# Kernel tuning notes

Hardware: AMD Instinct MI355X
Metric: run time of the kernel (lower is better)

The kernel has to match this reference:

```python
import jax, jax.numpy as jnp
import numpy as np

B, N, C, H, E = 16, 512, 128, 8, 131072
Nn = B * N
Dh = C // H
EPS = 1e-5


def setup_inputs() -> dict:
    key = jax.random.key(0)
    ks = jax.random.split(key, 16)
    s = C ** -0.5
    x = jax.random.normal(ks[0], (Nn, C), dtype=jnp.float32)
    edge_index = jax.random.randint(ks[1], (2, E), 0, Nn)
    batch = jnp.arange(Nn) // N  # B equal-sized graphs, sorted
    attn_bias = jax.random.normal(ks[2], (B, N, N, H), dtype=jnp.float32)
    return {
        "x": x,
        "edge_index": edge_index,
        "batch": batch,
        "attn_bias": attn_bias,
        "conv_w": jax.random.normal(ks[3], (C, C)) * s,
        "conv_b": jnp.zeros((C,)),
        "wq": jax.random.normal(ks[4], (C, C)) * s,
        "bq": jnp.zeros((C,)),
        "wk": jax.random.normal(ks[5], (C, C)) * s,
        "bk": jnp.zeros((C,)),
        "wv": jax.random.normal(ks[6], (C, C)) * s,
        "bv": jnp.zeros((C,)),
        "wo": jax.random.normal(ks[7], (C, C)) * s,
        "bo": jnp.zeros((C,)),
        "w1": jax.random.normal(ks[8], (C, 2 * C)) * s,
        "b1": jnp.zeros((2 * C,)),
        "w2": jax.random.normal(ks[9], (2 * C, C)) * (2 * C) ** -0.5,
        "b2": jnp.zeros((C,)),
        "g1": jnp.ones((C,)), "be1": jnp.zeros((C,)),
        "g2": jnp.ones((C,)), "be2": jnp.zeros((C,)),
        "g3": jnp.ones((C,)), "be3": jnp.zeros((C,)),
    }


def _bn(h, g, b):
    # BatchNorm1d over the node dimension (training-mode batch statistics)
    mu = h.mean(axis=0)
    var = h.var(axis=0)  # biased, matches torch normalization
    return g * (h - mu) * jax.lax.rsqrt(var + EPS) + b


def reference(x, edge_index, batch, attn_bias,
              conv_w, conv_b, wq, bq, wk, bk, wv, bv, wo, bo,
              w1, b1, w2, b2, g1, be1, g2, be2, g3, be3):
    n_nodes, ch = x.shape
    bsz, n_max, _, heads = attn_bias.shape
    dh = ch // heads

    # ---- GCN conv (self loops + symmetric norm) -> dropout(0) + residual + norm1
    loops = jnp.arange(n_nodes)
    src = jnp.concatenate([edge_index[0], loops])
    dst = jnp.concatenate([edge_index[1], loops])
    deg = jax.ops.segment_sum(jnp.ones_like(src, dtype=x.dtype), dst, num_segments=n_nodes)
    dinv = jax.lax.rsqrt(jnp.maximum(deg, 1.0))
    xw = x @ conv_w
    msg = xw[src] * (dinv[src] * dinv[dst])[:, None]
    hconv = jax.ops.segment_sum(msg, dst, num_segments=n_nodes) + conv_b
    h1 = _bn(hconv + x, g1, be1)

    # ---- dense batch (equal-sized sorted graphs -> pure reshape, mask all-valid)
    xd = x.reshape(bsz, n_max, ch)
    q = ((xd @ wq + bq) * (dh ** -0.5)).reshape(bsz, n_max, heads, dh)
    k = (xd @ wk + bk).reshape(bsz, n_max, heads, dh)
    v = (xd @ wv + bv).reshape(bsz, n_max, heads, dh)
    scores = jnp.einsum('bqhd,bkhd->bqkh', q, k) + attn_bias  # [B,N,N,H]
    probs = jax.nn.softmax(scores, axis=2)
    att = jnp.einsum('bqkh,bkhd->bqhd', probs, v).reshape(bsz, n_max, ch)
    att = att @ wo + bo
    h2 = _bn(att.reshape(n_nodes, ch) + x, g2, be2)

    # ---- combine branches, MLP with residual, norm3
    out = h1 + h2
    mlp = jax.nn.relu(out @ w1 + b1) @ w2 + b2
    return _bn(out + mlp, g3, be3)
```

## Files before the change

### kernel.cpp

```cpp
#include <hip/hip_runtime.h>
#include <cstddef>

#define NN 8192
#define CC 128


__global__ __launch_bounds__(256) void count_deg_int_k(const int* __restrict__ dst, int* degi, int E) {
  int i = blockIdx.x * 256 + threadIdx.x;
  if (i < E) atomicAdd(&degi[dst[i]], 1);
}

__global__ __launch_bounds__(256) void dinv_k(const int* __restrict__ degi, float* __restrict__ dinv, int n) {
  int i = blockIdx.x * 256 + threadIdx.x;
  if (i < n) dinv[i] = rsqrtf((float)(degi[i] + 1));
}

__global__ __launch_bounds__(256) void scan_k(const int* __restrict__ degi, int* __restrict__ rowstart,
                                              int* __restrict__ cursor) {
  __shared__ int partial[256];
  int t = threadIdx.x;
  int base = t * 32;
  int local[32];
  int s = 0;
#pragma unroll
  for (int i = 0; i < 32; ++i) { local[i] = s; s += degi[base + i]; }
  partial[t] = s;
  __syncthreads();
  for (int off = 1; off < 256; off <<= 1) {
    int v = (t >= off) ? partial[t - off] : 0;
    __syncthreads();
    partial[t] += v;
    __syncthreads();
  }
  int offset = partial[t] - s;
#pragma unroll
  for (int i = 0; i < 32; ++i) {
    rowstart[base + i] = offset + local[i];
    cursor[base + i] = offset + local[i];
  }
  if (t == 255) rowstart[NN] = offset + s;
}

__global__ __launch_bounds__(256) void bucket_k(const int* __restrict__ src, const int* __restrict__ dst,
    int* __restrict__ cursor, int* __restrict__ col, int E) {
  int e = blockIdx.x * 256 + threadIdx.x;
  if (e >= E) return;
  int d = dst[e];
  int pos = atomicAdd(&cursor[d], 1);
  col[pos] = src[e];
}

__global__ __launch_bounds__(256) void gather_k(const int* __restrict__ rowstart, const int* __restrict__ col,
    const float* __restrict__ xw, const float* __restrict__ dinv, const float* __restrict__ cb,
    const float* __restrict__ x, float* __restrict__ h1) {
  int d = blockIdx.x * 2 + (threadIdx.x >> 7);
  int c = threadIdx.x & 127;
  int j0 = rowstart[d], j1 = rowstart[d + 1];
  float dd = dinv[d];
  float sum = 0.f;
  int s_next = (j0 < j1) ? col[j0] : 0;
  for (int j = j0; j < j1; ++j) {
    int s = s_next;
    if (j + 1 < j1) s_next = col[j + 1];
    sum += xw[(size_t)s * CC + c] * dinv[s];
  }
  sum *= dd;
  int idx = d * CC + c;
  sum += xw[idx] * dd * dd;
  h1[idx] = sum + cb[c] + x[idx];
}


__global__ __launch_bounds__(256) void bn_stats_k(const float* __restrict__ X,
    float* __restrict__ sums, float* __restrict__ sumsq) {
  int t = threadIdx.x;
  int c = t & 127, rg = t >> 7;
  int r0 = blockIdx.x * 64;
  float s = 0.f, sq = 0.f;
  for (int i = 0; i < 32; ++i) {
    float v = X[(size_t)(r0 + rg + 2 * i) * CC + c];
    s += v; sq += v * v;
  }
  atomicAdd(&sums[c], s);
  atomicAdd(&sumsq[c], sq);
}

__global__ void bn_finalize_k(const float* sums, const float* sumsq, const float* g, const float* be,
                              float* scale, float* shift) {
  int c = threadIdx.x;
  float mu = sums[c] * (1.0f / NN);
  float var = sumsq[c] * (1.0f / NN) - mu * mu;
  float sc = g[c] * rsqrtf(var + 1e-5f);
  scale[c] = sc;
  shift[c] = be[c] - mu * sc;
}

__global__ __launch_bounds__(256) void combine_k(const float* __restrict__ h1, const float* __restrict__ h2,
    const float* __restrict__ sc0, const float* __restrict__ sh0,
    const float* __restrict__ sc1, const float* __restrict__ sh1, float* __restrict__ out) {
  int idx = blockIdx.x * 256 + threadIdx.x;
  int c = idx & 127;
  out[idx] = sc0[c] * h1[idx] + sh0[c] + sc1[c] * h2[idx] + sh1[c];
}

__global__ __launch_bounds__(256) void bn_apply_k(const float* __restrict__ h, const float* __restrict__ sc,
    const float* __restrict__ sh, float* __restrict__ out) {
  int idx = blockIdx.x * 256 + threadIdx.x;
  int c = idx & 127;
  out[idx] = sc[c] * h[idx] + sh[c];
}

__global__ __launch_bounds__(256) void gemm_k(const float* __restrict__ A, const float* __restrict__ W,
    const float* __restrict__ bias, const float* __restrict__ resid, float* __restrict__ out,
    int M, int N, int K, float scale, int relu) {
  __shared__ float As[64 * 128];
  __shared__ float Ws[128 * 64];
  int t = threadIdx.x;
  int ty = t >> 4, tx = t & 15;
  int row0 = blockIdx.x * 64, n0 = blockIdx.y * 64;
  float acc[4][4] = {};
  for (int kc = 0; kc < K; kc += 128) {
#pragma unroll
    for (int j = 0; j < 8; ++j) {
      int f = t + 256 * j;
      int r = f >> 5, c4 = f & 31;
      *(float4*)(As + r * 128 + c4 * 4) = *(const float4*)(A + (size_t)(row0 + r) * K + kc + c4 * 4);
    }
#pragma unroll
    for (int j = 0; j < 8; ++j) {
      int f = t + 256 * j;
      int kr = f >> 4, c4 = f & 15;
      *(float4*)(Ws + kr * 64 + c4 * 4) = *(const float4*)(W + (size_t)(kc + kr) * N + n0 + c4 * 4);
    }
    __syncthreads();
    for (int k0 = 0; k0 < 128; k0 += 4) {
      float a[4][4], b[4][4];
#pragma unroll
      for (int i = 0; i < 4; ++i) {
        float4 t4 = *(const float4*)(As + (4 * ty + i) * 128 + k0);
        a[i][0] = t4.x; a[i][1] = t4.y; a[i][2] = t4.z; a[i][3] = t4.w;
      }
#pragma unroll
      for (int kk = 0; kk < 4; ++kk) {
        float4 t4 = *(const float4*)(Ws + (k0 + kk) * 64 + 4 * tx);
        b[kk][0] = t4.x; b[kk][1] = t4.y; b[kk][2] = t4.z; b[kk][3] = t4.w;
      }
#pragma unroll
      for (int kk = 0; kk < 4; ++kk)
#pragma unroll
        for (int i = 0; i < 4; ++i)
#pragma unroll
          for (int j = 0; j < 4; ++j)
            acc[i][j] += a[i][kk] * b[kk][j];
    }
    __syncthreads();
  }
  float4 bv = make_float4(0.f, 0.f, 0.f, 0.f);
  if (bias) bv = *(const float4*)(bias + n0 + 4 * tx);
#pragma unroll
  for (int i = 0; i < 4; ++i) {
    float4 r;
    r.x = (acc[i][0] + bv.x) * scale;
    r.y = (acc[i][1] + bv.y) * scale;
    r.z = (acc[i][2] + bv.z) * scale;
    r.w = (acc[i][3] + bv.w) * scale;
    if (relu) { r.x = fmaxf(r.x, 0.f); r.y = fmaxf(r.y, 0.f); r.z = fmaxf(r.z, 0.f); r.w = fmaxf(r.w, 0.f); }
    size_t o = (size_t)(row0 + 4 * ty + i) * N + n0 + 4 * tx;
    if (resid) {
      float4 rv = *(const float4*)(resid + o);
      r.x += rv.x; r.y += rv.y; r.z += rv.z; r.w += rv.w;
    }
    *(float4*)(out + o) = r;
  }
}

__global__ __launch_bounds__(256) void attn_k(const float* __restrict__ Q, const float* __restrict__ K,
    const float* __restrict__ V, const float* __restrict__ bias, float* __restrict__ out) {
  __shared__ float Ks[64 * 128];
  __shared__ float Vs[64 * 128];
  const int t = threadIdx.x;
  const int b = blockIdx.x >> 4;
  const int qt = blockIdx.x & 15;
  const int q = t >> 3;
  const int h = t & 7;
  const int node = b * 512 + qt * 32 + q;

  float qf[16];
  {
    const float4* qp = (const float4*)(Q + (size_t)node * CC + h * 16);
    float4 q0 = qp[0], q1 = qp[1], q2 = qp[2], q3 = qp[3];
    qf[0] = q0.x; qf[1] = q0.y; qf[2] = q0.z; qf[3] = q0.w;
    qf[4] = q1.x; qf[5] = q1.y; qf[6] = q1.z; qf[7] = q1.w;
    qf[8] = q2.x; qf[9] = q2.y; qf[10] = q2.z; qf[11] = q2.w;
    qf[12] = q3.x; qf[13] = q3.y; qf[14] = q3.z; qf[15] = q3.w;
  }
  float m = -INFINITY, l = 0.f;
  float acc[16];
#pragma unroll
  for (int d = 0; d < 16; ++d) acc[d] = 0.f;

  const float* brow = bias + (size_t)node * 4096 + h;
  float bb_cur[8], bb_nxt[8];
#pragma unroll
  for (int j = 0; j < 8; ++j) bb_cur[j] = brow[j * 8];
#pragma unroll
  for (int j = 0; j < 8; ++j) bb_nxt[j] = 0.f;

  const size_t kbase = (size_t)b * 512 * CC;
  for (int kt = 0; kt < 8; ++kt) {
    __syncthreads();
#pragma unroll
    for (int j = 0; j < 8; ++j) {
      int f = t + 256 * j;
      int r = f >> 5, c4 = f & 31;
      *(float4*)(Ks + r * 128 + c4 * 4) = *(const float4*)(K + kbase + (size_t)(kt * 64 + r) * CC + c4 * 4);
      *(float4*)(Vs + r * 128 + c4 * 4) = *(const float4*)(V + kbase + (size_t)(kt * 64 + r) * CC + c4 * 4);
    }
    __syncthreads();
    for (int c = 0; c < 8; ++c) {
      int gc = kt * 8 + c;
      if (gc < 63) {
#pragma unroll
        for (int j = 0; j < 8; ++j) bb_nxt[j] = brow[(size_t)((gc + 1) * 8 + j) * 8];
      }
#pragma unroll
      for (int j = 0; j < 8; ++j) {
        int kk = c * 8 + j;
        const float4* kf = (const float4*)(Ks + kk * 128 + h * 16);
        float4 k0 = kf[0], k1 = kf[1], k2 = kf[2], k3 = kf[3];
        float s = bb_cur[j]
          + qf[0] * k0.x + qf[1] * k0.y + qf[2] * k0.z + qf[3] * k0.w
          + qf[4] * k1.x + qf[5] * k1.y + qf[6] * k1.z + qf[7] * k1.w
          + qf[8] * k2.x + qf[9] * k2.y + qf[10] * k2.z + qf[11] * k2.w
          + qf[12] * k3.x + qf[13] * k3.y + qf[14] * k3.z + qf[15] * k3.w;
        if (s > m) {
          float al = __expf(m - s);
          l *= al;
#pragma unroll
          for (int d = 0; d < 16; ++d) acc[d] *= al;
          m = s;
        }
        float p = __expf(s - m);
        l += p;
        const float4* vf = (const float4*)(Vs + kk * 128 + h * 16);
        float4 v0 = vf[0], v1 = vf[1], v2 = vf[2], v3 = vf[3];
        acc[0] += p * v0.x; acc[1] += p * v0.y; acc[2] += p * v0.z; acc[3] += p * v0.w;
        acc[4] += p * v1.x; acc[5] += p * v1.y; acc[6] += p * v1.z; acc[7] += p * v1.w;
        acc[8] += p * v2.x; acc[9] += p * v2.y; acc[10] += p * v2.z; acc[11] += p * v2.w;
        acc[12] += p * v3.x; acc[13] += p * v3.y; acc[14] += p * v3.z; acc[15] += p * v3.w;
      }
#pragma unroll
      for (int j = 0; j < 8; ++j) bb_cur[j] = bb_nxt[j];
    }
  }
  float inv = 1.f / l;
  float* op = out + (size_t)node * CC + h * 16;
  *(float4*)(op + 0)  = make_float4(acc[0] * inv, acc[1] * inv, acc[2] * inv, acc[3] * inv);
  *(float4*)(op + 4)  = make_float4(acc[4] * inv, acc[5] * inv, acc[6] * inv, acc[7] * inv);
  *(float4*)(op + 8)  = make_float4(acc[8] * inv, acc[9] * inv, acc[10] * inv, acc[11] * inv);
  *(float4*)(op + 12) = make_float4(acc[12] * inv, acc[13] * inv, acc[14] * inv, acc[15] * inv);
}


extern "C" void kernel_launch(void* const* d_in, const int* in_sizes, int n_in,
                              void* d_out, int out_size, void* d_ws, size_t ws_size,
                              hipStream_t stream) {
  const float* x      = (const float*)d_in[0];
  const int*   ei     = (const int*)d_in[1];
  const float* bias   = (const float*)d_in[3];
  const float* conv_w = (const float*)d_in[4];
  const float* conv_b = (const float*)d_in[5];
  const float* wq = (const float*)d_in[6];
  const float* bq = (const float*)d_in[7];
  const float* wk = (const float*)d_in[8];
  const float* bk = (const float*)d_in[9];
  const float* wv = (const float*)d_in[10];
  const float* bv = (const float*)d_in[11];
  const float* wo = (const float*)d_in[12];
  const float* bo = (const float*)d_in[13];
  const float* w1 = (const float*)d_in[14];
  const float* b1 = (const float*)d_in[15];
  const float* w2 = (const float*)d_in[16];
  const float* b2 = (const float*)d_in[17];
  const float* g1 = (const float*)d_in[18];
  const float* be1 = (const float*)d_in[19];
  const float* g2 = (const float*)d_in[20];
  const float* be2 = (const float*)d_in[21];
  const float* g3 = (const float*)d_in[22];
  const float* be3 = (const float*)d_in[23];
  int E = in_sizes[1] / 2;

  float* ws = (float*)d_ws;
  const size_t NC = (size_t)NN * CC;
  float* xw     = ws;
  float* h1pre  = ws + NC;
  float* qb     = ws + 2 * NC;
  float* kb     = ws + 3 * NC;
  float* vb     = ws + 4 * NC;
  float* h2pre  = ws + 5 * NC;
  float* outbuf = ws + 6 * NC;
  float* hid    = ws + 2 * NC;
  float* h3pre  = ws + 4 * NC;
  float* st     = ws + 7 * NC;
  float* dinv   = ws + 7 * NC + 1536;
  int*   degi     = (int*)(ws + 7 * NC + 1536 + NN);
  int*   rowstart = degi + NN;
  int*   cursor   = rowstart + NN + 1;
  int*   col      = cursor + NN;

  hipMemsetAsync(degi, 0, NN * sizeof(int), stream);
  hipMemsetAsync(st, 0, 1536 * sizeof(float), stream);

  count_deg_int_k<<<(E + 255) / 256, 256, 0, stream>>>(ei + E, degi, E);
  dinv_k<<<NN / 256, 256, 0, stream>>>(degi, dinv, NN);
  scan_k<<<1, 256, 0, stream>>>(degi, rowstart, cursor);
  bucket_k<<<(E + 255) / 256, 256, 0, stream>>>(ei, ei + E, cursor, col, E);
  gemm_k<<<dim3(NN / 64, 2), 256, 0, stream>>>(x, conv_w, nullptr, nullptr, xw, NN, CC, CC, 1.f, 0);
  gather_k<<<NN / 2, 256, 0, stream>>>(rowstart, col, xw, dinv, conv_b, x, h1pre);
  bn_stats_k<<<NN / 64, 256, 0, stream>>>(h1pre, st + 0, st + 128);

  gemm_k<<<dim3(NN / 64, 2), 256, 0, stream>>>(x, wq, bq, nullptr, qb, NN, CC, CC, 0.25f, 0);
  gemm_k<<<dim3(NN / 64, 2), 256, 0, stream>>>(x, wk, bk, nullptr, kb, NN, CC, CC, 1.f, 0);
  gemm_k<<<dim3(NN / 64, 2), 256, 0, stream>>>(x, wv, bv, nullptr, vb, NN, CC, CC, 1.f, 0);
  attn_k<<<256, 256, 0, stream>>>(qb, kb, vb, bias, xw);
  gemm_k<<<dim3(NN / 64, 2), 256, 0, stream>>>(xw, wo, bo, x, h2pre, NN, CC, CC, 1.f, 0);
  bn_stats_k<<<NN / 64, 256, 0, stream>>>(h2pre, st + 256, st + 384);

  bn_finalize_k<<<1, 128, 0, stream>>>(st + 0, st + 128, g1, be1, st + 768, st + 896);
  bn_finalize_k<<<1, 128, 0, stream>>>(st + 256, st + 384, g2, be2, st + 1024, st + 1152);
  combine_k<<<NC / 256, 256, 0, stream>>>(h1pre, h2pre, st + 768, st + 896, st + 1024, st + 1152, outbuf);
  gemm_k<<<dim3(NN / 64, 4), 256, 0, stream>>>(outbuf, w1, b1, nullptr, hid, NN, 2 * CC, CC, 1.f, 1);
  gemm_k<<<dim3(NN / 64, 2), 256, 0, stream>>>(hid, w2, b2, outbuf, h3pre, NN, CC, 2 * CC, 1.f, 0);
  bn_stats_k<<<NN / 64, 256, 0, stream>>>(h3pre, st + 512, st + 640);
  bn_finalize_k<<<1, 128, 0, stream>>>(st + 512, st + 640, g3, be3, st + 1280, st + 1408);
  bn_apply_k<<<NC / 256, 256, 0, stream>>>(h3pre, st + 1280, st + 1408, (float*)d_out);
}
```

Baseline: 446.3 us.

## Split attention over key halves with two queries per thread and padded LDS

```diff
diff --git a/kernel.cpp b/kernel.cpp
--- a/kernel.cpp
+++ b/kernel.cpp
@@ -113,7 +113,7 @@
 __global__ __launch_bounds__(256) void gemm_k(const float* __restrict__ A, const float* __restrict__ W,
     const float* __restrict__ bias, const float* __restrict__ resid, float* __restrict__ out,
     int M, int N, int K, float scale, int relu) {
-  __shared__ float As[64 * 128];
+  __shared__ float As[64 * 132];
   __shared__ float Ws[128 * 64];
   int t = threadIdx.x;
   int ty = t >> 4, tx = t & 15;
@@ -124,7 +124,7 @@
     for (int j = 0; j < 8; ++j) {
       int f = t + 256 * j;
       int r = f >> 5, c4 = f & 31;
-      *(float4*)(As + r * 128 + c4 * 4) = *(const float4*)(A + (size_t)(row0 + r) * K + kc + c4 * 4);
+      *(float4*)(As + r * 132 + c4 * 4) = *(const float4*)(A + (size_t)(row0 + r) * K + kc + c4 * 4);
     }
 #pragma unroll
     for (int j = 0; j < 8; ++j) {
@@ -137,7 +137,7 @@
       float a[4][4], b[4][4];
 #pragma unroll
       for (int i = 0; i < 4; ++i) {
-        float4 t4 = *(const float4*)(As + (4 * ty + i) * 128 + k0);
+        float4 t4 = *(const float4*)(As + (4 * ty + i) * 132 + k0);
         a[i][0] = t4.x; a[i][1] = t4.y; a[i][2] = t4.z; a[i][3] = t4.w;
       }
 #pragma unroll
@@ -174,91 +174,140 @@
   }
 }
 
-__global__ __launch_bounds__(256) void attn_k(const float* __restrict__ Q, const float* __restrict__ K,
-    const float* __restrict__ V, const float* __restrict__ bias, float* __restrict__ out) {
-  __shared__ float Ks[64 * 128];
-  __shared__ float Vs[64 * 128];
+#define ROWS 160
+__global__ __launch_bounds__(128) void attn_k(const float* __restrict__ Q, const float* __restrict__ K,
+    const float* __restrict__ V, const float* __restrict__ bias,
+    float* __restrict__ accA, float* __restrict__ accB, float* __restrict__ ml) {
+  __shared__ float Ks[64 * ROWS];
+  __shared__ float Vs[64 * ROWS];
   const int t = threadIdx.x;
   const int b = blockIdx.x >> 4;
   const int qt = blockIdx.x & 15;
-  const int q = t >> 3;
+  const int s = blockIdx.y;
+  const int qp = t >> 3;
   const int h = t & 7;
-  const int node = b * 512 + qt * 32 + q;
-
-  float qf[16];
+  const int node0 = b * 512 + qt * 32 + qp * 2;
+
+  float qf0[16], qf1[16];
   {
-    const float4* qp = (const float4*)(Q + (size_t)node * CC + h * 16);
-    float4 q0 = qp[0], q1 = qp[1], q2 = qp[2], q3 = qp[3];
-    qf[0] = q0.x; qf[1] = q0.y; qf[2] = q0.z; qf[3] = q0.w;
-    qf[4] = q1.x; qf[5] = q1.y; qf[6] = q1.z; qf[7] = q1.w;
-    qf[8] = q2.x; qf[9] = q2.y; qf[10] = q2.z; qf[11] = q2.w;
-    qf[12] = q3.x; qf[13] = q3.y; qf[14] = q3.z; qf[15] = q3.w;
-  }
-  float m = -INFINITY, l = 0.f;
-  float acc[16];
-#pragma unroll
-  for (int d = 0; d < 16; ++d) acc[d] = 0.f;
-
-  const float* brow = bias + (size_t)node * 4096 + h;
-  float bb_cur[8], bb_nxt[8];
-#pragma unroll
-  for (int j = 0; j < 8; ++j) bb_cur[j] = brow[j * 8];
-#pragma unroll
-  for (int j = 0; j < 8; ++j) bb_nxt[j] = 0.f;
-
-  const size_t kbase = (size_t)b * 512 * CC;
-  for (int kt = 0; kt < 8; ++kt) {
-    __syncthreads();
-#pragma unroll
-    for (int j = 0; j < 8; ++j) {
-      int f = t + 256 * j;
+    const float4* qa = (const float4*)(Q + (size_t)node0 * CC + h * 16);
+    const float4* qb = (const float4*)(Q + (size_t)(node0 + 1) * CC + h * 16);
+#pragma unroll
+    for (int i = 0; i < 4; ++i) {
+      float4 a = qa[i], c = qb[i];
+      qf0[4*i] = a.x; qf0[4*i+1] = a.y; qf0[4*i+2] = a.z; qf0[4*i+3] = a.w;
+      qf1[4*i] = c.x; qf1[4*i+1] = c.y; qf1[4*i+2] = c.z; qf1[4*i+3] = c.w;
+    }
+  }
+  float m0 = -INFINITY, l0 = 0.f, m1 = -INFINITY, l1 = 0.f;
+  float ac0[16], ac1[16];
+#pragma unroll
+  for (int d = 0; d < 16; ++d) { ac0[d] = 0.f; ac1[d] = 0.f; }
+
+  const float* brow0 = bias + (size_t)node0 * 4096 + h;
+  const float* brow1 = brow0 + 4096;
+  const int kbase0 = s * 256;
+  float b0c[8], b1c[8], b0n[8], b1n[8];
+#pragma unroll
+  for (int j = 0; j < 8; ++j) {
+    b0c[j] = brow0[(size_t)(kbase0 + j) * 8];
+    b1c[j] = brow1[(size_t)(kbase0 + j) * 8];
+  }
+
+  const size_t kvbase = (size_t)b * 512 * CC + (size_t)kbase0 * CC;
+  for (int kt = 0; kt < 4; ++kt) {
+    __syncthreads();
+#pragma unroll
+    for (int j = 0; j < 16; ++j) {
+      int f = t + 128 * j;
       int r = f >> 5, c4 = f & 31;
-      *(float4*)(Ks + r * 128 + c4 * 4) = *(const float4*)(K + kbase + (size_t)(kt * 64 + r) * CC + c4 * 4);
-      *(float4*)(Vs + r * 128 + c4 * 4) = *(const float4*)(V + kbase + (size_t)(kt * 64 + r) * CC + c4 * 4);
+      int lo = r * ROWS + (c4 >> 2) * 20 + (c4 & 3) * 4;
+      size_t go = kvbase + (size_t)(kt * 64 + r) * CC + c4 * 4;
+      *(float4*)(Ks + lo) = *(const float4*)(K + go);
+      *(float4*)(Vs + lo) = *(const float4*)(V + go);
     }
     __syncthreads();
     for (int c = 0; c < 8; ++c) {
-      int gc = kt * 8 + c;
-      if (gc < 63) {
-#pragma unroll
-        for (int j = 0; j < 8; ++j) bb_nxt[j] = brow[(size_t)((gc + 1) * 8 + j) * 8];
+      int lc = kt * 8 + c;
+      if (lc < 31) {
+#pragma unroll
+        for (int j = 0; j < 8; ++j) {
+          size_t o = (size_t)(kbase0 + (lc + 1) * 8 + j) * 8;
+          b0n[j] = brow0[o];
+          b1n[j] = brow1[o];
+        }
       }
 #pragma unroll
       for (int j = 0; j < 8; ++j) {
         int kk = c * 8 + j;
-        const float4* kf = (const float4*)(Ks + kk * 128 + h * 16);
+        const float4* kf = (const float4*)(Ks + kk * ROWS + h * 20);
         float4 k0 = kf[0], k1 = kf[1], k2 = kf[2], k3 = kf[3];
-        float s = bb_cur[j]
-          + qf[0] * k0.x + qf[1] * k0.y + qf[2] * k0.z + qf[3] * k0.w
-          + qf[4] * k1.x + qf[5] * k1.y + qf[6] * k1.z + qf[7] * k1.w
-          + qf[8] * k2.x + qf[9] * k2.y + qf[10] * k2.z + qf[11] * k2.w
-          + qf[12] * k3.x + qf[13] * k3.y + qf[14] * k3.z + qf[15] * k3.w;
-        if (s > m) {
-          float al = __expf(m - s);
-          l *= al;
-#pragma unroll
-          for (int d = 0; d < 16; ++d) acc[d] *= al;
-          m = s;
+        float kv[16] = {k0.x,k0.y,k0.z,k0.w,k1.x,k1.y,k1.z,k1.w,
+                        k2.x,k2.y,k2.z,k2.w,k3.x,k3.y,k3.z,k3.w};
+        float s0 = b0c[j], s1 = b1c[j];
+#pragma unroll
+        for (int d = 0; d < 16; ++d) { s0 += qf0[d] * kv[d]; s1 += qf1[d] * kv[d]; }
+        if (s0 > m0) {
+          float al = __expf(m0 - s0);
+          l0 *= al;
+#pragma unroll
+          for (int d = 0; d < 16; ++d) ac0[d] *= al;
+          m0 = s0;
         }
-        float p = __expf(s - m);
-        l += p;
-        const float4* vf = (const float4*)(Vs + kk * 128 + h * 16);
+        if (s1 > m1) {
+          float al = __expf(m1 - s1);
+          l1 *= al;
+#pragma unroll
+          for (int d = 0; d < 16; ++d) ac1[d] *= al;
+          m1 = s1;
+        }
+        float p0 = __expf(s0 - m0);
+        float p1 = __expf(s1 - m1);
+        l0 += p0; l1 += p1;
+        const float4* vf = (const float4*)(Vs + kk * ROWS + h * 20);
         float4 v0 = vf[0], v1 = vf[1], v2 = vf[2], v3 = vf[3];
-        acc[0] += p * v0.x; acc[1] += p * v0.y; acc[2] += p * v0.z; acc[3] += p * v0.w;
-        acc[4] += p * v1.x; acc[5] += p * v1.y; acc[6] += p * v1.z; acc[7] += p * v1.w;
-        acc[8] += p * v2.x; acc[9] += p * v2.y; acc[10] += p * v2.z; acc[11] += p * v2.w;
-        acc[12] += p * v3.x; acc[13] += p * v3.y; acc[14] += p * v3.z; acc[15] += p * v3.w;
+        float vv[16] = {v0.x,v0.y,v0.z,v0.w,v1.x,v1.y,v1.z,v1.w,
+                        v2.x,v2.y,v2.z,v2.w,v3.x,v3.y,v3.z,v3.w};
+#pragma unroll
+        for (int d = 0; d < 16; ++d) { ac0[d] += p0 * vv[d]; ac1[d] += p1 * vv[d]; }
       }
 #pragma unroll
-      for (int j = 0; j < 8; ++j) bb_cur[j] = bb_nxt[j];
-    }
-  }
-  float inv = 1.f / l;
-  float* op = out + (size_t)node * CC + h * 16;
-  *(float4*)(op + 0)  = make_float4(acc[0] * inv, acc[1] * inv, acc[2] * inv, acc[3] * inv);
-  *(float4*)(op + 4)  = make_float4(acc[4] * inv, acc[5] * inv, acc[6] * inv, acc[7] * inv);
-  *(float4*)(op + 8)  = make_float4(acc[8] * inv, acc[9] * inv, acc[10] * inv, acc[11] * inv);
-  *(float4*)(op + 12) = make_float4(acc[12] * inv, acc[13] * inv, acc[14] * inv, acc[15] * inv);
+      for (int j = 0; j < 8; ++j) { b0c[j] = b0n[j]; b1c[j] = b1n[j]; }
+    }
+  }
+  float* dst = s ? accB : accA;
+  float* o0 = dst + (size_t)node0 * CC + h * 16;
+  float* o1 = o0 + CC;
+#pragma unroll
+  for (int i = 0; i < 4; ++i) {
+    *(float4*)(o0 + 4 * i) = make_float4(ac0[4*i], ac0[4*i+1], ac0[4*i+2], ac0[4*i+3]);
+    *(float4*)(o1 + 4 * i) = make_float4(ac1[4*i], ac1[4*i+1], ac1[4*i+2], ac1[4*i+3]);
+  }
+  float* mlp = ml + (size_t)s * 65536 * 2;
+  int i0 = (node0 * 8 + h) * 2;
+  mlp[i0] = m0; mlp[i0 + 1] = l0;
+  mlp[i0 + 16] = m1; mlp[i0 + 17] = l1;
+}
+
+__global__ __launch_bounds__(256) void attn_merge_k(const float* __restrict__ accA, const float* __restrict__ accB,
+    const float* __restrict__ ml, float* __restrict__ out) {
+  int i = blockIdx.x * 256 + threadIdx.x;
+  int node = i >> 3, h = i & 7;
+  float m0 = ml[i * 2], l0 = ml[i * 2 + 1];
+  float m1 = ml[131072 + i * 2], l1 = ml[131072 + i * 2 + 1];
+  float M = fmaxf(m0, m1);
+  float a0 = __expf(m0 - M), a1 = __expf(m1 - M);
+  float inv = 1.f / (l0 * a0 + l1 * a1);
+  a0 *= inv; a1 *= inv;
+  const float4* pa = (const float4*)(accA + (size_t)node * CC + h * 16);
+  const float4* pb = (const float4*)(accB + (size_t)node * CC + h * 16);
+  float4* po = (float4*)(out + (size_t)node * CC + h * 16);
+#pragma unroll
+  for (int k = 0; k < 4; ++k) {
+    float4 x = pa[k], y = pb[k];
+    po[k] = make_float4(x.x * a0 + y.x * a1, x.y * a0 + y.y * a1,
+                        x.z * a0 + y.z * a1, x.w * a0 + y.w * a1);
+  }
 }
 
 
@@ -307,6 +356,7 @@
   int*   rowstart = degi + NN;
   int*   cursor   = rowstart + NN + 1;
   int*   col      = cursor + NN;
+  float* mlbuf    = (float*)(col + E);
 
   hipMemsetAsync(degi, 0, NN * sizeof(int), stream);
   hipMemsetAsync(st, 0, 1536 * sizeof(float), stream);
@@ -322,7 +372,8 @@
   gemm_k<<<dim3(NN / 64, 2), 256, 0, stream>>>(x, wq, bq, nullptr, qb, NN, CC, CC, 0.25f, 0);
   gemm_k<<<dim3(NN / 64, 2), 256, 0, stream>>>(x, wk, bk, nullptr, kb, NN, CC, CC, 1.f, 0);
   gemm_k<<<dim3(NN / 64, 2), 256, 0, stream>>>(x, wv, bv, nullptr, vb, NN, CC, CC, 1.f, 0);
-  attn_k<<<256, 256, 0, stream>>>(qb, kb, vb, bias, xw);
+  attn_k<<<dim3(256, 2), 128, 0, stream>>>(qb, kb, vb, bias, h2pre, outbuf, mlbuf);
+  attn_merge_k<<<65536 / 256, 256, 0, stream>>>(h2pre, outbuf, mlbuf, xw);
   gemm_k<<<dim3(NN / 64, 2), 256, 0, stream>>>(xw, wo, bo, x, h2pre, NN, CC, CC, 1.f, 0);
   bn_stats_k<<<NN / 64, 256, 0, stream>>>(h2pre, st + 256, st + 384);
 
```

Result: no change. 452.2 us (+1.3%).
